# Performance work log

Hardware: AMD Instinct MI355X
Metric: run time of the kernel (lower is better)

Reference implementation:

```python
import jax, jax.numpy as jnp
import numpy as np

N, E, C, S, G = 20000, 320000, 32, 64, 64
NRAD, HRAD, OUTS, HHEAD, NSH, NL = 8, 64, 16, 64, 9, 2
RCUT = 5.0
LIDX = np.repeat(np.arange(3), [1, 3, 5])  # l index of each of the 9 sh components


def _sph_harm(u):
    # real spherical harmonics up to l=2 on unit vectors, [E,3] -> [E,9]
    x, y, z = u[:, 0], u[:, 1], u[:, 2]
    s3 = jnp.sqrt(jnp.asarray(3.0, u.dtype))
    return jnp.stack([
        jnp.ones_like(x), x, y, z,
        s3 * x * y, s3 * y * z, 0.5 * (3 * z * z - 1.0), s3 * x * z,
        0.5 * s3 * (x * x - y * y)
    ], axis=1)


def _bessel(r):
    # Bessel radial basis with smooth polynomial envelope, [E] -> [E, NRAD]
    n = jnp.arange(1, NRAD + 1, dtype=r.dtype)
    rs = jnp.clip(r, 1e-6, None)[:, None]
    u = jnp.clip(r / RCUT, 0.0, 1.0)
    env = ((1 - u) ** 2 * (1 + 2 * u))[:, None]
    return jnp.sqrt(2.0 / RCUT) * jnp.sin(n * jnp.pi * rs / RCUT) / rs * env


def setup_inputs() -> dict:
    key = jax.random.key(0)
    ks = jax.random.split(key, 16)
    return {
        'vectors': jax.random.normal(ks[0], (E, 3), jnp.float32),
        'node_species': jax.random.randint(ks[1], (N,), 0, S),
        'senders': jax.random.randint(ks[2], (E,), 0, N),
        'receivers': jax.random.randint(ks[3], (E,), 0, N),
        'graph_id': jnp.sort(jax.random.randint(ks[4], (N,), 0, G)),
        'species_embed': jax.random.normal(ks[5], (S, C), jnp.float32) * 0.1,
        'w_r1': jax.random.normal(ks[6], (NRAD, HRAD), jnp.float32) / np.sqrt(NRAD),
        'b_r1': jnp.zeros((HRAD,), jnp.float32),
        'w_r2': jax.random.normal(ks[7], (NL, HRAD, 3 * C), jnp.float32) / np.sqrt(HRAD),
        'w_mix': jax.random.normal(ks[8], (NL, 3, C, C), jnp.float32) / np.sqrt(C),
        'w_sc': jax.random.normal(ks[9], (NL, S, C, C), jnp.float32) / np.sqrt(C),
        'w_readout': jax.random.normal(ks[10], (C, OUTS), jnp.float32) / np.sqrt(C),
        'ln_gamma': jnp.ones((OUTS,), jnp.float32),
        'ln_beta': jnp.zeros((OUTS,), jnp.float32),
        'w_h1': jax.random.normal(ks[11], (OUTS, HHEAD), jnp.float32) / np.sqrt(OUTS),
        'b_h1': jnp.zeros((HHEAD,), jnp.float32),
        'w_h2': jax.random.normal(ks[12], (HHEAD, 1), jnp.float32) / np.sqrt(HHEAD),
        'b_h2': jnp.zeros((1,), jnp.float32),
        'scale': jnp.ones((), jnp.float32),
        'shift': jnp.zeros((), jnp.float32),
    }


def reference(vectors, node_species, senders, receivers, graph_id, species_embed,
              w_r1, b_r1, w_r2, w_mix, w_sc, w_readout, ln_gamma, ln_beta,
              w_h1, b_h1, w_h2, b_h2, scale, shift):
    lidx = jnp.asarray(LIDX)
    # nan-safe edge norms and unit vectors (safe_norm in source)
    r2 = jnp.sum(vectors ** 2, axis=-1)
    r = jnp.where(r2 == 0, 0.0, jnp.sqrt(jnp.where(r2 == 0, 1.0, r2)))
    u = vectors / jnp.where(r == 0, 1.0, r)[:, None]
    sh = _sph_harm(u)                                  # [E,9]
    rad = jax.nn.silu(_bessel(r) @ w_r1 + b_r1)        # [E,HRAD] radial MLP
    h = species_embed[node_species]                    # [N,C] node embedding
    for li in range(NL):
        # per-edge, per-l, per-channel radial weights, expanded to the 9 sh components
        rw = (rad @ w_r2[li]).reshape(E, 3, C)[:, lidx, :]     # [E,9,C]
        # tensor-product message: radial * sender scalars * Y_lm
        msg = sh[:, :, None] * rw * h[senders][:, None, :]     # [E,9,C]
        agg = jax.ops.segment_sum(msg, receivers, num_segments=N)  # [N,9,C]
        # per-irrep (per-l) channel-mixing linear
        mixed = jnp.einsum('nmc,mcd->nmd', agg, w_mix[li][lidx])   # [N,9,C]
        # species-dependent self-connection on the scalar (l=0) channel
        sc = jnp.einsum('nc,ncd->nd', h, w_sc[li][node_species])   # [N,C]
        h = mixed[:, 0, :] + sc + h                                # residual
    readout = h @ w_readout                            # [N,OUTS] (last-block readout)
    mu = jnp.mean(readout, axis=-1, keepdims=True)
    var = jnp.var(readout, axis=-1, keepdims=True)
    nrm = (readout - mu) * jax.lax.rsqrt(var + 1e-6) * ln_gamma + ln_beta
    node_out = (jax.nn.gelu(nrm @ w_h1 + b_h1) @ w_h2 + b_h2)[:, 0]  # [N]
    gsum = jax.ops.segment_sum(node_out, graph_id, num_segments=G)
    cnt = jax.ops.segment_sum(jnp.ones((N,), node_out.dtype), graph_id, num_segments=G)
    gmean = gsum / jnp.clip(cnt, 1.0, None)            # segment-mean node2graph
    return (gmean * scale + shift)[:, None]            # [G,1]
```

## Files before the change

kernel.cpp:

```cpp
#include <hip/hip_runtime.h>
#include <cstdint>
#include <cmath>

#define NE 320000
#define NN 20000
#define NG 64

typedef __attribute__((ext_vector_type(8))) short s16x8;
typedef __attribute__((ext_vector_type(4))) float f32x4;

static __device__ __forceinline__ unsigned short f32_to_bf16(float x) {
    unsigned int u = __float_as_uint(x);
    u = (u + 0x7fffu + ((u >> 16) & 1u)) >> 16;
    return (unsigned short)u;
}
static __device__ __forceinline__ float bf16_to_f32(unsigned short h) {
    return __uint_as_float(((unsigned int)h) << 16);
}

__global__ __launch_bounds__(256) void setup_kernel(
    const int* __restrict__ spec, const float* __restrict__ emb,
    float* __restrict__ h,
    const float* __restrict__ w_r2,
    unsigned short* __restrict__ wt_hi, unsigned short* __restrict__ wt_lo,
    int* __restrict__ deg, float* __restrict__ gzero, int N)
{
    int t = blockIdx.x * 256 + threadIdx.x;
    if (t < N * 32) h[t] = emb[spec[t >> 5] * 32 + (t & 31)];
    if (t < 4096) {
        int c = t >> 6, k = t & 63;
        float v = w_r2[(c >= 32 ? 6144 : 0) + k * 96 + (c & 31)];
        unsigned short hb = f32_to_bf16(v);
        wt_hi[t] = hb;
        wt_lo[t] = f32_to_bf16(v - bf16_to_f32(hb));
    }
    if (t < N) deg[t] = 0;
    if (t < 128) gzero[t] = 0.0f;
}

__global__ __launch_bounds__(256) void edge_gemm_kernel(
    const float* __restrict__ vectors,
    const float* __restrict__ w_r1,
    const float* __restrict__ b_r1,
    const unsigned short* __restrict__ wt_hi,
    const unsigned short* __restrict__ wt_lo,
    float* __restrict__ rw0_0,
    float* __restrict__ rw0_1)
{
    __shared__ __attribute__((aligned(16))) short sh_hi[256 * 72];
    __shared__ __attribute__((aligned(16))) short sh_lo[256 * 72];

    const int tid = threadIdx.x;
    const int e = blockIdx.x * 256 + tid;

    float x = vectors[3 * e + 0];
    float y = vectors[3 * e + 1];
    float z = vectors[3 * e + 2];
    float r2 = x * x + y * y + z * z;
    float r = (r2 == 0.0f) ? 0.0f : sqrtf(r2);
    float rs = fmaxf(r, 1e-6f);
    float u = fminf(r * 0.2f, 1.0f);
    float env = (1.0f - u) * (1.0f - u) * (1.0f + 2.0f * u);
    float pref = 0.6324555320336759f * env / rs;
    float theta = 0.6283185307179586f * rs;

    float s1 = __sinf(theta), c1 = __cosf(theta);
    float twoc = 2.0f * c1;
    float b[8];
    {
        float sp = 0.0f, s = s1;
#pragma unroll
        for (int n = 0; n < 8; ++n) {
            b[n] = pref * s;
            float nx = twoc * s - sp;
            sp = s; s = nx;
        }
    }

#pragma unroll
    for (int j0 = 0; j0 < 64; j0 += 8) {
        short hibuf[8], lobuf[8];
#pragma unroll
        for (int jj = 0; jj < 8; ++jj) {
            int j = j0 + jj;
            float pre = b_r1[j];
#pragma unroll
            for (int n = 0; n < 8; ++n) pre = fmaf(b[n], w_r1[n * 64 + j], pre);
            float rj = pre * __builtin_amdgcn_rcpf(1.0f + __expf(-pre));
            unsigned short hb = f32_to_bf16(rj);
            float lov = rj - bf16_to_f32(hb);
            hibuf[jj] = (short)hb;
            lobuf[jj] = (short)f32_to_bf16(lov);
        }
        *(s16x8*)&sh_hi[tid * 72 + j0] =
            (s16x8){hibuf[0],hibuf[1],hibuf[2],hibuf[3],hibuf[4],hibuf[5],hibuf[6],hibuf[7]};
        *(s16x8*)&sh_lo[tid * 72 + j0] =
            (s16x8){lobuf[0],lobuf[1],lobuf[2],lobuf[3],lobuf[4],lobuf[5],lobuf[6],lobuf[7]};
    }

    __syncthreads();

    const int wv = tid >> 6;
    const int l = tid & 63;
    const int lrow = l & 15;
    const int lk = l >> 4;

    s16x8 Bhi[4][2], Blo[4][2];
#pragma unroll
    for (int ct = 0; ct < 4; ++ct)
#pragma unroll
        for (int kt = 0; kt < 2; ++kt) {
            int col = ct * 16 + lrow;
            int kof = kt * 32 + lk * 8;
            Bhi[ct][kt] = *(const s16x8*)(wt_hi + col * 64 + kof);
            Blo[ct][kt] = *(const s16x8*)(wt_lo + col * 64 + kof);
        }

    f32x4 acc[4][4];
#pragma unroll
    for (int rt = 0; rt < 4; ++rt)
#pragma unroll
        for (int ct = 0; ct < 4; ++ct) acc[rt][ct] = (f32x4){0.f, 0.f, 0.f, 0.f};

#pragma unroll
    for (int rt = 0; rt < 4; ++rt) {
        int row = wv * 64 + rt * 16 + lrow;
#pragma unroll
        for (int kt = 0; kt < 2; ++kt) {
            s16x8 ahi = *(const s16x8*)&sh_hi[row * 72 + kt * 32 + lk * 8];
            s16x8 alo = *(const s16x8*)&sh_lo[row * 72 + kt * 32 + lk * 8];
#pragma unroll
            for (int ct = 0; ct < 4; ++ct) {
                acc[rt][ct] = __builtin_amdgcn_mfma_f32_16x16x32_bf16(ahi, Bhi[ct][kt], acc[rt][ct], 0, 0, 0);
                acc[rt][ct] = __builtin_amdgcn_mfma_f32_16x16x32_bf16(alo, Bhi[ct][kt], acc[rt][ct], 0, 0, 0);
                acc[rt][ct] = __builtin_amdgcn_mfma_f32_16x16x32_bf16(ahi, Blo[ct][kt], acc[rt][ct], 0, 0, 0);
            }
        }
    }

#pragma unroll
    for (int rt = 0; rt < 4; ++rt) {
#pragma unroll
        for (int ct = 0; ct < 4; ++ct) {
            int ebase = blockIdx.x * 256 + wv * 64 + rt * 16 + lk * 4;
            int col = ct * 16 + lrow;
            float* base = (col < 32) ? (rw0_0 + col) : (rw0_1 + (col - 32));
#pragma unroll
            for (int rr = 0; rr < 4; ++rr)
                base[(size_t)(ebase + rr) * 32] = acc[rt][ct][rr];
        }
    }
}

__global__ __launch_bounds__(256) void count_kernel(
    const int* __restrict__ recv, int* __restrict__ deg, int E)
{
    int e = blockIdx.x * 256 + threadIdx.x;
    if (e < E) atomicAdd(&deg[recv[e]], 1);
}

__global__ __launch_bounds__(256) void scanA_kernel(
    const int* __restrict__ deg, int* __restrict__ scanned,
    int* __restrict__ bsum, int N)
{
    __shared__ int lds[256];
    int tid = threadIdx.x;
    int i = blockIdx.x * 256 + tid;
    int v = (i < N) ? deg[i] : 0;
    lds[tid] = v;
    __syncthreads();
    for (int off = 1; off < 256; off <<= 1) {
        int t = (tid >= off) ? lds[tid - off] : 0;
        __syncthreads();
        lds[tid] += t;
        __syncthreads();
    }
    if (i < N) scanned[i] = lds[tid] - v;
    if (tid == 255) bsum[blockIdx.x] = lds[tid];
}

__global__ __launch_bounds__(128) void scanB_kernel(int* __restrict__ bsum, int nb)
{
    __shared__ int wtot;
    int tid = threadIdx.x;
    int lane = tid & 63;
    int orig = (tid < nb) ? bsum[tid] : 0;
    int v = orig;
#pragma unroll
    for (int off = 1; off < 64; off <<= 1) {
        int u = __shfl_up(v, off);
        if (lane >= off) v += u;
    }
    if (tid == 63) wtot = v;
    __syncthreads();
    if (tid >= 64) v += wtot;
    if (tid < nb) bsum[tid] = v - orig;
}

__global__ __launch_bounds__(256) void scanC_kernel(
    const int* __restrict__ scanned, const int* __restrict__ bsum,
    int* __restrict__ rowstart, int* __restrict__ cursor, int N, int E)
{
    int i = blockIdx.x * 256 + threadIdx.x;
    if (i < N) {
        int rs = scanned[i] + bsum[blockIdx.x];
        rowstart[i] = rs;
        cursor[i] = rs;
    }
    if (i == 0) rowstart[N] = E;
}

__global__ __launch_bounds__(256) void scatter_kernel(
    const int* __restrict__ recv, const int* __restrict__ snd,
    int* __restrict__ cursor, int2* __restrict__ eids, int E)
{
    int e = blockIdx.x * 256 + threadIdx.x;
    if (e < E) {
        int slot = atomicAdd(&cursor[recv[e]], 1);
        eids[slot] = make_int2(e, snd[e]);
    }
}

__global__ __launch_bounds__(256) void agg_update_kernel(
    const float* __restrict__ rw0, const float* __restrict__ h_in,
    const int* __restrict__ rowstart, const int2* __restrict__ eids,
    const int* __restrict__ spec,
    const float* __restrict__ w_mix0,
    const float* __restrict__ w_sc_l,
    float* __restrict__ h_out, int N)
{
    int t = blockIdx.x * 256 + threadIdx.x;
    int n = t >> 5, c = t & 31;
    int lane = threadIdx.x & 63;
    int half = lane & 32;

    int s0 = rowstart[n], s1 = rowstart[n + 1];
    float acc = 0.0f;
    int k = s0;
    for (; k + 1 < s1; k += 2) {
        int2 a = eids[k];
        int2 b = eids[k + 1];
        float r1 = rw0[(size_t)a.x * 32 + c];
        float h1 = h_in[(size_t)a.y * 32 + c];
        float r2 = rw0[(size_t)b.x * 32 + c];
        float h2 = h_in[(size_t)b.y * 32 + c];
        acc = fmaf(r1, h1, acc);
        acc = fmaf(r2, h2, acc);
    }
    if (k < s1) {
        int2 a = eids[k];
        acc = fmaf(rw0[(size_t)a.x * 32 + c], h_in[(size_t)a.y * 32 + c], acc);
    }

    float hv = h_in[t];
    int sp = spec[n];
    const float* wsc = w_sc_l + sp * 1024;
    float outv = hv;
#pragma unroll
    for (int cp = 0; cp < 32; ++cp) {
        float av  = __shfl(acc, half + cp);
        float hvb = __shfl(hv,  half + cp);
        outv = fmaf(av,  w_mix0[cp * 32 + c], outv);
        outv = fmaf(hvb, wsc[cp * 32 + c], outv);
    }
    h_out[t] = outv;
}

__global__ __launch_bounds__(256) void readout_kernel(
    const float* __restrict__ h, const int* __restrict__ gid_arr,
    const float* __restrict__ w_ro,
    const float* __restrict__ gamma, const float* __restrict__ beta,
    const float* __restrict__ w_h1, const float* __restrict__ b_h1,
    const float* __restrict__ w_h2, const float* __restrict__ b_h2,
    float* __restrict__ gsum, float* __restrict__ gcnt, int N)
{
    int t = blockIdx.x * 256 + threadIdx.x;
    int lane = threadIdx.x & 63;
    bool active = t < N;

    float val = 0.0f;
    int gid = -1;
    if (active) {
        gid = gid_arr[t];
        const float* hr = h + (size_t)t * 32;
        float ro[16];
#pragma unroll
        for (int o = 0; o < 16; ++o) ro[o] = 0.0f;
#pragma unroll
        for (int c = 0; c < 32; ++c) {
            float hv = hr[c];
#pragma unroll
            for (int o = 0; o < 16; ++o) ro[o] = fmaf(hv, w_ro[c * 16 + o], ro[o]);
        }
        float mu = 0.0f;
#pragma unroll
        for (int o = 0; o < 16; ++o) mu += ro[o];
        mu *= (1.0f / 16.0f);
        float var = 0.0f;
#pragma unroll
        for (int o = 0; o < 16; ++o) { float d = ro[o] - mu; var = fmaf(d, d, var); }
        var *= (1.0f / 16.0f);
        float inv = rsqrtf(var + 1e-6f);
        float nrm[16];
#pragma unroll
        for (int o = 0; o < 16; ++o) nrm[o] = (ro[o] - mu) * inv * gamma[o] + beta[o];

        float outv = b_h2[0];
        for (int j = 0; j < 64; ++j) {
            float a = b_h1[j];
#pragma unroll
            for (int o = 0; o < 16; ++o) a = fmaf(nrm[o], w_h1[o * 64 + j], a);
            float g = 0.5f * a * (1.0f + tanhf(0.7978845608028654f * (a + 0.044715f * a * a * a)));
            outv = fmaf(g, w_h2[j], outv);
        }
        val = outv;
    }
    float cval = active ? 1.0f : 0.0f;

#pragma unroll
    for (int off = 1; off < 64; off <<= 1) {
        float v = __shfl_down(val, off);
        float cv = __shfl_down(cval, off);
        int g = __shfl_down(gid, off);
        if (lane + off < 64 && g == gid) { val += v; cval += cv; }
    }
    int gprev = __shfl_up(gid, 1);
    bool head = (lane == 0) || (gprev != gid);
    if (active && head) {
        atomicAdd(&gsum[gid], val);
        atomicAdd(&gcnt[gid], cval);
    }
}

__global__ void finalize_kernel(const float* __restrict__ gsum,
                                const float* __restrict__ gcnt,
                                const float* __restrict__ scale,
                                const float* __restrict__ shift,
                                float* __restrict__ out, int G)
{
    int g = blockIdx.x * blockDim.x + threadIdx.x;
    if (g < G) out[g] = gsum[g] / fmaxf(gcnt[g], 1.0f) * scale[0] + shift[0];
}

extern "C" void kernel_launch(void* const* d_in, const int* in_sizes, int n_in,
                              void* d_out, int out_size, void* d_ws, size_t ws_size,
                              hipStream_t stream)
{
    const float* vectors       = (const float*)d_in[0];
    const int*   node_species  = (const int*)d_in[1];
    const int*   senders       = (const int*)d_in[2];
    const int*   receivers     = (const int*)d_in[3];
    const int*   graph_id      = (const int*)d_in[4];
    const float* species_embed = (const float*)d_in[5];
    const float* w_r1          = (const float*)d_in[6];
    const float* b_r1          = (const float*)d_in[7];
    const float* w_r2          = (const float*)d_in[8];
    const float* w_mix         = (const float*)d_in[9];
    const float* w_sc          = (const float*)d_in[10];
    const float* w_ro          = (const float*)d_in[11];
    const float* ln_gamma      = (const float*)d_in[12];
    const float* ln_beta       = (const float*)d_in[13];
    const float* w_h1          = (const float*)d_in[14];
    const float* b_h1          = (const float*)d_in[15];
    const float* w_h2          = (const float*)d_in[16];
    const float* b_h2          = (const float*)d_in[17];
    const float* scale         = (const float*)d_in[18];
    const float* shift         = (const float*)d_in[19];
    float* out = (float*)d_out;

    const int E = NE, N = NN, G = NG;
    const int NB = (N + 255) / 256;

    float* ws    = (float*)d_ws;
    float* rw0_0 = ws;
    float* rw0_1 = rw0_0 + (size_t)E * 32;
    float* hA    = rw0_1 + (size_t)E * 32;
    float* hB    = hA + (size_t)N * 32;
    float* gsum  = hB + (size_t)N * 32;
    float* gcnt  = gsum + G;
    unsigned short* wt_hi = (unsigned short*)(gcnt + G);
    unsigned short* wt_lo = wt_hi + 4096;
    int* deg      = (int*)(wt_lo + 4096);
    int* scanned  = deg + N;
    int* bsum     = scanned + N;
    int* rowstart = bsum + 128;
    int* cursor   = rowstart + N + 1;
    int2* eids    = (int2*)(cursor + N + 1);

    setup_kernel<<<(N * 32 + 255) / 256, 256, 0, stream>>>(
        node_species, species_embed, hA, w_r2, wt_hi, wt_lo, deg, gsum, N);

    count_kernel<<<(E + 255) / 256, 256, 0, stream>>>(receivers, deg, E);
    scanA_kernel<<<NB, 256, 0, stream>>>(deg, scanned, bsum, N);
    scanB_kernel<<<1, 128, 0, stream>>>(bsum, NB);
    scanC_kernel<<<NB, 256, 0, stream>>>(scanned, bsum, rowstart, cursor, N, E);
    scatter_kernel<<<(E + 255) / 256, 256, 0, stream>>>(receivers, senders, cursor, eids, E);

    edge_gemm_kernel<<<E / 256, 256, 0, stream>>>(
        vectors, w_r1, b_r1, wt_hi, wt_lo, rw0_0, rw0_1);

    float* hin = hA;
    float* hout = hB;
    const float* rw0s[2] = {rw0_0, rw0_1};
    for (int li = 0; li < 2; ++li) {
        agg_update_kernel<<<(N * 32) / 256, 256, 0, stream>>>(
            rw0s[li], hin, rowstart, eids, node_species,
            w_mix + li * 3072, w_sc + li * 65536, hout, N);
        float* tmp = hin; hin = hout; hout = tmp;
    }

    readout_kernel<<<(N + 255) / 256, 256, 0, stream>>>(
        hin, graph_id, w_ro, ln_gamma, ln_beta, w_h1, b_h1, w_h2, b_h2, gsum, gcnt, N);
    finalize_kernel<<<1, 64, 0, stream>>>(gsum, gcnt, scale, shift, out, G);
}
```

Before: 156.2 us.

## Fuse degree count into edge GEMM, store radial weights as fp16, fuse readout

The degree-count atomics move into the edge GEMM kernel. The three-kernel scan becomes a single-block 1024-thread scan. The per-edge radial weights are staged through LDS, converted to fp16 and written with coalesced 16-byte stores, which halves that traffic and its gather reads. The second aggregation layer is fused with the readout, LayerNorm, MLP head and graph-sum, so each node is handled by 32 lanes instead of one thread. This cuts launch count and memory traffic, at the cost of fp16 rounding in the radial weights and a serial single-block scan.

```diff
diff --git a/kernel.cpp b/kernel.cpp
--- a/kernel.cpp
+++ b/kernel.cpp
@@ -1,4 +1,5 @@
 #include <hip/hip_runtime.h>
+#include <hip/hip_fp16.h>
 #include <cstdint>
 #include <cmath>
 
@@ -23,10 +24,10 @@
     float* __restrict__ h,
     const float* __restrict__ w_r2,
     unsigned short* __restrict__ wt_hi, unsigned short* __restrict__ wt_lo,
-    int* __restrict__ deg, float* __restrict__ gzero, int N)
+    int* __restrict__ deg, float* __restrict__ gz)
 {
     int t = blockIdx.x * 256 + threadIdx.x;
-    if (t < N * 32) h[t] = emb[spec[t >> 5] * 32 + (t & 31)];
+    if (t < NN * 32) h[t] = emb[spec[t >> 5] * 32 + (t & 31)];
     if (t < 4096) {
         int c = t >> 6, k = t & 63;
         float v = w_r2[(c >= 32 ? 6144 : 0) + k * 96 + (c & 31)];
@@ -34,8 +35,8 @@
         wt_hi[t] = hb;
         wt_lo[t] = f32_to_bf16(v - bf16_to_f32(hb));
     }
-    if (t < N) deg[t] = 0;
-    if (t < 128) gzero[t] = 0.0f;
+    if (t < NN) deg[t] = 0;
+    if (t < 128) gz[t] = 0.0f;
 }
 
 __global__ __launch_bounds__(256) void edge_gemm_kernel(
@@ -44,14 +45,18 @@
     const float* __restrict__ b_r1,
     const unsigned short* __restrict__ wt_hi,
     const unsigned short* __restrict__ wt_lo,
-    float* __restrict__ rw0_0,
-    float* __restrict__ rw0_1)
+    const int* __restrict__ recv,
+    int* __restrict__ deg,
+    __half* __restrict__ rw0_0,
+    __half* __restrict__ rw0_1)
 {
     __shared__ __attribute__((aligned(16))) short sh_hi[256 * 72];
     __shared__ __attribute__((aligned(16))) short sh_lo[256 * 72];
 
     const int tid = threadIdx.x;
     const int e = blockIdx.x * 256 + tid;
+
+    atomicAdd(&deg[recv[e]], 1);
 
     float x = vectors[3 * e + 0];
     float y = vectors[3 * e + 1];
@@ -138,197 +143,181 @@
         }
     }
 
-#pragma unroll
-    for (int rt = 0; rt < 4; ++rt) {
+    __syncthreads();
+    __half* stg = (__half*)sh_hi;
+#pragma unroll
+    for (int rt = 0; rt < 4; ++rt)
 #pragma unroll
         for (int ct = 0; ct < 4; ++ct) {
-            int ebase = blockIdx.x * 256 + wv * 64 + rt * 16 + lk * 4;
             int col = ct * 16 + lrow;
-            float* base = (col < 32) ? (rw0_0 + col) : (rw0_1 + (col - 32));
-#pragma unroll
-            for (int rr = 0; rr < 4; ++rr)
-                base[(size_t)(ebase + rr) * 32] = acc[rt][ct][rr];
-        }
-    }
-}
-
-__global__ __launch_bounds__(256) void count_kernel(
-    const int* __restrict__ recv, int* __restrict__ deg, int E)
-{
-    int e = blockIdx.x * 256 + threadIdx.x;
-    if (e < E) atomicAdd(&deg[recv[e]], 1);
-}
-
-__global__ __launch_bounds__(256) void scanA_kernel(
-    const int* __restrict__ deg, int* __restrict__ scanned,
-    int* __restrict__ bsum, int N)
-{
-    __shared__ int lds[256];
-    int tid = threadIdx.x;
-    int i = blockIdx.x * 256 + tid;
-    int v = (i < N) ? deg[i] : 0;
-    lds[tid] = v;
+#pragma unroll
+            for (int rr = 0; rr < 4; ++rr) {
+                int erow = wv * 64 + rt * 16 + lk * 4 + rr;
+                stg[erow * 72 + col] = __float2half_rn(acc[rt][ct][rr]);
+            }
+        }
     __syncthreads();
-    for (int off = 1; off < 256; off <<= 1) {
-        int t = (tid >= off) ? lds[tid - off] : 0;
+    {
+        const s16x8* src = (const s16x8*)&sh_hi[tid * 72];
+        size_t eb = (size_t)e * 32;
+        s16x8* d0 = (s16x8*)(rw0_0 + eb);
+        s16x8* d1 = (s16x8*)(rw0_1 + eb);
+        d0[0] = src[0]; d0[1] = src[1]; d0[2] = src[2]; d0[3] = src[3];
+        d1[0] = src[4]; d1[1] = src[5]; d1[2] = src[6]; d1[3] = src[7];
+    }
+}
+
+__global__ __launch_bounds__(1024) void scan_kernel(
+    const int* __restrict__ deg,
+    int* __restrict__ rowstart, int* __restrict__ cursor)
+{
+    __shared__ int tsum[1024];
+    const int tid = threadIdx.x;
+    const int PER = (NN + 1023) / 1024;
+    const int base = tid * PER;
+
+    int s = 0;
+    for (int i = 0; i < PER; ++i) {
+        int idx = base + i;
+        if (idx < NN) s += deg[idx];
+    }
+    tsum[tid] = s;
+    __syncthreads();
+    for (int off = 1; off < 1024; off <<= 1) {
+        int v = (tid >= off) ? tsum[tid - off] : 0;
         __syncthreads();
-        lds[tid] += t;
+        tsum[tid] += v;
         __syncthreads();
     }
-    if (i < N) scanned[i] = lds[tid] - v;
-    if (tid == 255) bsum[blockIdx.x] = lds[tid];
-}
-
-__global__ __launch_bounds__(128) void scanB_kernel(int* __restrict__ bsum, int nb)
-{
-    __shared__ int wtot;
-    int tid = threadIdx.x;
-    int lane = tid & 63;
-    int orig = (tid < nb) ? bsum[tid] : 0;
-    int v = orig;
-#pragma unroll
-    for (int off = 1; off < 64; off <<= 1) {
-        int u = __shfl_up(v, off);
-        if (lane >= off) v += u;
-    }
-    if (tid == 63) wtot = v;
-    __syncthreads();
-    if (tid >= 64) v += wtot;
-    if (tid < nb) bsum[tid] = v - orig;
-}
-
-__global__ __launch_bounds__(256) void scanC_kernel(
-    const int* __restrict__ scanned, const int* __restrict__ bsum,
-    int* __restrict__ rowstart, int* __restrict__ cursor, int N, int E)
-{
-    int i = blockIdx.x * 256 + threadIdx.x;
-    if (i < N) {
-        int rs = scanned[i] + bsum[blockIdx.x];
-        rowstart[i] = rs;
-        cursor[i] = rs;
-    }
-    if (i == 0) rowstart[N] = E;
+    int run = tsum[tid] - s;
+    for (int i = 0; i < PER; ++i) {
+        int idx = base + i;
+        if (idx < NN) {
+            rowstart[idx] = run;
+            cursor[idx] = run;
+            run += deg[idx];
+        }
+    }
+    if (tid == 1023) rowstart[NN] = NE;
 }
 
 __global__ __launch_bounds__(256) void scatter_kernel(
     const int* __restrict__ recv, const int* __restrict__ snd,
-    int* __restrict__ cursor, int2* __restrict__ eids, int E)
+    int* __restrict__ cursor, int2* __restrict__ eids)
 {
     int e = blockIdx.x * 256 + threadIdx.x;
-    if (e < E) {
-        int slot = atomicAdd(&cursor[recv[e]], 1);
-        eids[slot] = make_int2(e, snd[e]);
-    }
-}
-
-__global__ __launch_bounds__(256) void agg_update_kernel(
-    const float* __restrict__ rw0, const float* __restrict__ h_in,
+    int slot = atomicAdd(&cursor[recv[e]], 1);
+    eids[slot] = make_int2(e, snd[e]);
+}
+
+__device__ __forceinline__ float agg_update_val(
+    const __half* __restrict__ rw0h, const float* __restrict__ hin,
     const int* __restrict__ rowstart, const int2* __restrict__ eids,
     const int* __restrict__ spec,
-    const float* __restrict__ w_mix0,
-    const float* __restrict__ w_sc_l,
-    float* __restrict__ h_out, int N)
-{
-    int t = blockIdx.x * 256 + threadIdx.x;
-    int n = t >> 5, c = t & 31;
-    int lane = threadIdx.x & 63;
-    int half = lane & 32;
-
+    const float* __restrict__ wmix0, const float* __restrict__ wscl,
+    int t, int n, int c, int half)
+{
     int s0 = rowstart[n], s1 = rowstart[n + 1];
     float acc = 0.0f;
     int k = s0;
     for (; k + 1 < s1; k += 2) {
         int2 a = eids[k];
-        int2 b = eids[k + 1];
-        float r1 = rw0[(size_t)a.x * 32 + c];
-        float h1 = h_in[(size_t)a.y * 32 + c];
-        float r2 = rw0[(size_t)b.x * 32 + c];
-        float h2 = h_in[(size_t)b.y * 32 + c];
+        int2 bb = eids[k + 1];
+        float r1 = __half2float(rw0h[(size_t)a.x * 32 + c]);
+        float h1 = hin[(size_t)a.y * 32 + c];
+        float r2 = __half2float(rw0h[(size_t)bb.x * 32 + c]);
+        float h2 = hin[(size_t)bb.y * 32 + c];
         acc = fmaf(r1, h1, acc);
         acc = fmaf(r2, h2, acc);
     }
     if (k < s1) {
         int2 a = eids[k];
-        acc = fmaf(rw0[(size_t)a.x * 32 + c], h_in[(size_t)a.y * 32 + c], acc);
-    }
-
-    float hv = h_in[t];
-    int sp = spec[n];
-    const float* wsc = w_sc_l + sp * 1024;
+        acc = fmaf(__half2float(rw0h[(size_t)a.x * 32 + c]),
+                   hin[(size_t)a.y * 32 + c], acc);
+    }
+
+    float hv = hin[t];
+    const float* wsc = wscl + spec[n] * 1024;
     float outv = hv;
 #pragma unroll
     for (int cp = 0; cp < 32; ++cp) {
         float av  = __shfl(acc, half + cp);
         float hvb = __shfl(hv,  half + cp);
-        outv = fmaf(av,  w_mix0[cp * 32 + c], outv);
+        outv = fmaf(av,  wmix0[cp * 32 + c], outv);
         outv = fmaf(hvb, wsc[cp * 32 + c], outv);
     }
-    h_out[t] = outv;
-}
-
-__global__ __launch_bounds__(256) void readout_kernel(
-    const float* __restrict__ h, const int* __restrict__ gid_arr,
+    return outv;
+}
+
+__global__ __launch_bounds__(256) void agg_update_kernel(
+    const __half* __restrict__ rw0h, const float* __restrict__ hin,
+    const int* __restrict__ rowstart, const int2* __restrict__ eids,
+    const int* __restrict__ spec,
+    const float* __restrict__ wmix0, const float* __restrict__ wscl,
+    float* __restrict__ hout)
+{
+    int t = blockIdx.x * 256 + threadIdx.x;
+    int n = t >> 5, c = t & 31;
+    int half = (threadIdx.x & 63) & 32;
+    hout[t] = agg_update_val(rw0h, hin, rowstart, eids, spec, wmix0, wscl,
+                             t, n, c, half);
+}
+
+__global__ __launch_bounds__(256) void agg_readout_kernel(
+    const __half* __restrict__ rw0h, const float* __restrict__ hin,
+    const int* __restrict__ rowstart, const int2* __restrict__ eids,
+    const int* __restrict__ spec,
+    const float* __restrict__ wmix0, const float* __restrict__ wscl,
+    const int* __restrict__ gid_arr,
     const float* __restrict__ w_ro,
     const float* __restrict__ gamma, const float* __restrict__ beta,
     const float* __restrict__ w_h1, const float* __restrict__ b_h1,
     const float* __restrict__ w_h2, const float* __restrict__ b_h2,
-    float* __restrict__ gsum, float* __restrict__ gcnt, int N)
+    float* __restrict__ gsum, float* __restrict__ gcnt)
 {
     int t = blockIdx.x * 256 + threadIdx.x;
-    int lane = threadIdx.x & 63;
-    bool active = t < N;
-
-    float val = 0.0f;
-    int gid = -1;
-    if (active) {
-        gid = gid_arr[t];
-        const float* hr = h + (size_t)t * 32;
-        float ro[16];
-#pragma unroll
-        for (int o = 0; o < 16; ++o) ro[o] = 0.0f;
-#pragma unroll
-        for (int c = 0; c < 32; ++c) {
-            float hv = hr[c];
-#pragma unroll
-            for (int o = 0; o < 16; ++o) ro[o] = fmaf(hv, w_ro[c * 16 + o], ro[o]);
-        }
-        float mu = 0.0f;
-#pragma unroll
-        for (int o = 0; o < 16; ++o) mu += ro[o];
-        mu *= (1.0f / 16.0f);
-        float var = 0.0f;
-#pragma unroll
-        for (int o = 0; o < 16; ++o) { float d = ro[o] - mu; var = fmaf(d, d, var); }
-        var *= (1.0f / 16.0f);
-        float inv = rsqrtf(var + 1e-6f);
-        float nrm[16];
-#pragma unroll
-        for (int o = 0; o < 16; ++o) nrm[o] = (ro[o] - mu) * inv * gamma[o] + beta[o];
-
-        float outv = b_h2[0];
-        for (int j = 0; j < 64; ++j) {
-            float a = b_h1[j];
-#pragma unroll
-            for (int o = 0; o < 16; ++o) a = fmaf(nrm[o], w_h1[o * 64 + j], a);
-            float g = 0.5f * a * (1.0f + tanhf(0.7978845608028654f * (a + 0.044715f * a * a * a)));
-            outv = fmaf(g, w_h2[j], outv);
-        }
-        val = outv;
-    }
-    float cval = active ? 1.0f : 0.0f;
-
-#pragma unroll
-    for (int off = 1; off < 64; off <<= 1) {
-        float v = __shfl_down(val, off);
-        float cv = __shfl_down(cval, off);
-        int g = __shfl_down(gid, off);
-        if (lane + off < 64 && g == gid) { val += v; cval += cv; }
-    }
-    int gprev = __shfl_up(gid, 1);
-    bool head = (lane == 0) || (gprev != gid);
-    if (active && head) {
-        atomicAdd(&gsum[gid], val);
-        atomicAdd(&gcnt[gid], cval);
+    int n = t >> 5, c = t & 31;
+    int half = (threadIdx.x & 63) & 32;
+
+    float outv = agg_update_val(rw0h, hin, rowstart, eids, spec, wmix0, wscl,
+                                t, n, c, half);
+
+    int o = c & 15;
+    float ro = 0.0f;
+#pragma unroll
+    for (int cp = 0; cp < 32; ++cp) {
+        float hb = __shfl(outv, half + cp);
+        ro = fmaf(hb, w_ro[cp * 16 + o], ro);
+    }
+    float ssum = ro;
+#pragma unroll
+    for (int m = 1; m < 16; m <<= 1) ssum += __shfl_xor(ssum, m);
+    float mu = ssum * (1.0f / 16.0f);
+    float d = ro - mu;
+    float vs = d * d;
+#pragma unroll
+    for (int m = 1; m < 16; m <<= 1) vs += __shfl_xor(vs, m);
+    float inv = rsqrtf(vs * (1.0f / 16.0f) + 1e-6f);
+    float nrm = d * inv * gamma[o] + beta[o];
+
+    int j1 = c, j2 = c + 32;
+    float a1 = b_h1[j1], a2 = b_h1[j2];
+#pragma unroll
+    for (int oo = 0; oo < 16; ++oo) {
+        float nv = __shfl(nrm, half + oo);
+        a1 = fmaf(nv, w_h1[oo * 64 + j1], a1);
+        a2 = fmaf(nv, w_h1[oo * 64 + j2], a2);
+    }
+    float g1 = 0.5f * a1 * (1.0f + tanhf(0.7978845608028654f * (a1 + 0.044715f * a1 * a1 * a1)));
+    float g2 = 0.5f * a2 * (1.0f + tanhf(0.7978845608028654f * (a2 + 0.044715f * a2 * a2 * a2)));
+    float partial = fmaf(g1, w_h2[j1], g2 * w_h2[j2]);
+#pragma unroll
+    for (int m = 1; m < 32; m <<= 1) partial += __shfl_xor(partial, m);
+
+    if (c == 0) {
+        int gid = gid_arr[n];
+        atomicAdd(&gsum[gid], partial + b_h2[0]);
+        atomicAdd(&gcnt[gid], 1.0f);
     }
 }
 
@@ -336,10 +325,10 @@
                                 const float* __restrict__ gcnt,
                                 const float* __restrict__ scale,
                                 const float* __restrict__ shift,
-                                float* __restrict__ out, int G)
-{
-    int g = blockIdx.x * blockDim.x + threadIdx.x;
-    if (g < G) out[g] = gsum[g] / fmaxf(gcnt[g], 1.0f) * scale[0] + shift[0];
+                                float* __restrict__ out)
+{
+    int g = threadIdx.x;
+    if (g < NG) out[g] = gsum[g] / fmaxf(gcnt[g], 1.0f) * scale[0] + shift[0];
 }
 
 extern "C" void kernel_launch(void* const* d_in, const int* in_sizes, int n_in,
@@ -368,48 +357,35 @@
     const float* shift         = (const float*)d_in[19];
     float* out = (float*)d_out;
 
-    const int E = NE, N = NN, G = NG;
-    const int NB = (N + 255) / 256;
-
-    float* ws    = (float*)d_ws;
-    float* rw0_0 = ws;
-    float* rw0_1 = rw0_0 + (size_t)E * 32;
-    float* hA    = rw0_1 + (size_t)E * 32;
-    float* hB    = hA + (size_t)N * 32;
-    float* gsum  = hB + (size_t)N * 32;
-    float* gcnt  = gsum + G;
-    unsigned short* wt_hi = (unsigned short*)(gcnt + G);
+    __half* rw0_0 = (__half*)d_ws;
+    __half* rw0_1 = rw0_0 + (size_t)NE * 32;
+    float* hA     = (float*)(rw0_1 + (size_t)NE * 32);
+    float* hB     = hA + (size_t)NN * 32;
+    float* gsum   = hB + (size_t)NN * 32;
+    float* gcnt   = gsum + NG;
+    unsigned short* wt_hi = (unsigned short*)(gcnt + NG);
     unsigned short* wt_lo = wt_hi + 4096;
     int* deg      = (int*)(wt_lo + 4096);
-    int* scanned  = deg + N;
-    int* bsum     = scanned + N;
-    int* rowstart = bsum + 128;
-    int* cursor   = rowstart + N + 1;
-    int2* eids    = (int2*)(cursor + N + 1);
-
-    setup_kernel<<<(N * 32 + 255) / 256, 256, 0, stream>>>(
-        node_species, species_embed, hA, w_r2, wt_hi, wt_lo, deg, gsum, N);
-
-    count_kernel<<<(E + 255) / 256, 256, 0, stream>>>(receivers, deg, E);
-    scanA_kernel<<<NB, 256, 0, stream>>>(deg, scanned, bsum, N);
-    scanB_kernel<<<1, 128, 0, stream>>>(bsum, NB);
-    scanC_kernel<<<NB, 256, 0, stream>>>(scanned, bsum, rowstart, cursor, N, E);
-    scatter_kernel<<<(E + 255) / 256, 256, 0, stream>>>(receivers, senders, cursor, eids, E);
-
-    edge_gemm_kernel<<<E / 256, 256, 0, stream>>>(
-        vectors, w_r1, b_r1, wt_hi, wt_lo, rw0_0, rw0_1);
-
-    float* hin = hA;
-    float* hout = hB;
-    const float* rw0s[2] = {rw0_0, rw0_1};
-    for (int li = 0; li < 2; ++li) {
-        agg_update_kernel<<<(N * 32) / 256, 256, 0, stream>>>(
-            rw0s[li], hin, rowstart, eids, node_species,
-            w_mix + li * 3072, w_sc + li * 65536, hout, N);
-        float* tmp = hin; hin = hout; hout = tmp;
-    }
-
-    readout_kernel<<<(N + 255) / 256, 256, 0, stream>>>(
-        hin, graph_id, w_ro, ln_gamma, ln_beta, w_h1, b_h1, w_h2, b_h2, gsum, gcnt, N);
-    finalize_kernel<<<1, 64, 0, stream>>>(gsum, gcnt, scale, shift, out, G);
-}
+    int* rowstart = deg + NN;
+    int* cursor   = rowstart + NN + 1;
+    int2* eids    = (int2*)(cursor + NN + 1);
+
+    setup_kernel<<<(NN * 32 + 255) / 256, 256, 0, stream>>>(
+        node_species, species_embed, hA, w_r2, wt_hi, wt_lo, deg, gsum);
+
+    edge_gemm_kernel<<<NE / 256, 256, 0, stream>>>(
+        vectors, w_r1, b_r1, wt_hi, wt_lo, receivers, deg, rw0_0, rw0_1);
+
+    scan_kernel<<<1, 1024, 0, stream>>>(deg, rowstart, cursor);
+
+    scatter_kernel<<<NE / 256, 256, 0, stream>>>(receivers, senders, cursor, eids);
+
+    agg_update_kernel<<<(NN * 32) / 256, 256, 0, stream>>>(
+        rw0_0, hA, rowstart, eids, node_species, w_mix, w_sc, hB);
+
+    agg_readout_kernel<<<(NN * 32) / 256, 256, 0, stream>>>(
+        rw0_1, hB, rowstart, eids, node_species, w_mix + 3072, w_sc + 65536,
+        graph_id, w_ro, ln_gamma, ln_beta, w_h1, b_h1, w_h2, b_h2, gsum, gcnt);
+
+    finalize_kernel<<<1, 64, 0, stream>>>(gsum, gcnt, scale, shift, out);
+}
```

New measurement: 303.5 us. 94.3% more time.
